# Kernel tuning notes

Hardware: AMD Instinct MI355X
Metric: run time of the kernel (lower is better)

Reference implementation:

```python
import jax, jax.numpy as jnp
import numpy as np

CL = 32      # config.cl (latent width)
NOBJ = 32    # config.num_obj
N = 1024     # batch


def _linear_params(key, fan_in, fan_out):
    w = jax.random.normal(key, (fan_in, fan_out), dtype=jnp.float32) / np.sqrt(fan_in)
    b = jnp.full((fan_out,), 0.1, dtype=jnp.float32)
    return w, b


def setup_inputs() -> dict:
    key = jax.random.key(0)
    keys = jax.random.split(key, 16)
    inp = {"s": jax.random.normal(keys[0], (N, NOBJ, CL // 2), dtype=jnp.float32)}
    specs = [
        ("state_enc", [(CL // 2, CL)]),
        ("self", [(CL, CL), (CL, CL)]),
        ("rel", [(2 * CL + 1, 2 * CL), (2 * CL, CL), (CL, CL)]),
        ("att", [(2 * CL + 1, 2 * CL), (2 * CL, CL), (CL, 1)]),
        ("aff", [(CL, CL), (CL, CL), (CL, CL)]),
        ("out", [(2 * CL, CL), (CL, CL)]),
    ]
    k = 1
    for name, shapes in specs:
        for j, (fi, fo) in enumerate(shapes):
            w, b = _linear_params(keys[k], fi, fo)
            k += 1
            if len(shapes) == 1:
                inp[name + "_w"], inp[name + "_b"] = w, b
            else:
                inp[name + "_w" + str(j)], inp[name + "_b" + str(j)] = w, b
    inp["core_idx"] = 0
    return inp


def _forward(s, state_enc_w, state_enc_b,
             self_w0, self_b0, self_w1, self_b1,
             rel_w0, rel_b0, rel_w1, rel_b1, rel_w2, rel_b2,
             att_w0, att_b0, att_w1, att_b1, att_w2, att_b2,
             aff_w0, aff_b0, aff_w1, aff_b1, aff_w2, aff_b2,
             out_w0, out_b0, out_w1, out_b1):
    # state encoding; keep raw (x, y) positions in the first 2 channels
    enc = s @ state_enc_w + state_enc_b                      # (n, o, cl)
    s2 = jnp.concatenate([s[..., :2], enc[..., 2:]], axis=-1)  # (n, o, cl)

    # self dynamics (residual MLP)
    h1 = jax.nn.relu(s2 @ self_w0 + self_b0)
    self_dyn = h1 @ self_w1 + self_b1 + h1                   # (n, o, cl)

    # pairwise squared distance over first two channels
    pos = s2[..., :2]
    diff = pos[:, :, None, :] - pos[:, None, :, :]           # (n, o, o, 2)
    dist = jnp.sum(diff * diff, axis=-1)                     # (n, o, o)

    # first layer of the edge MLPs applied to cat(obj_i, obj_j, dist) without
    # materializing the (n, o, o, 2cl+1) concat: split weight into W_i|W_j|w_d
    def pair_first(W, b):
        a = s2 @ W[:CL]                                      # (n, o, H)
        c = s2 @ W[CL:2 * CL]                                # (n, o, H)
        return a[:, :, None, :] + c[:, None, :, :] + dist[..., None] * W[2 * CL] + b

    # relation core (residual on last layer)
    rel1 = jax.nn.relu(pair_first(rel_w0, rel_b0))           # (n, o, o, 2cl)
    rel2 = jax.nn.relu(rel1 @ rel_w1 + rel_b1)               # (n, o, o, cl)
    rel_f = rel2 @ rel_w2 + rel_b2 + rel2                    # (n, o, o, cl)

    # attention net -> exp (unnormalized attention)
    att = jax.nn.relu(pair_first(att_w0, att_b0))
    att = jax.nn.relu(att @ att_w1 + att_b1)
    att = jnp.exp(att @ att_w2 + att_b2)                     # (n, o, o, 1)

    diag_mask = (1.0 - jnp.eye(NOBJ, dtype=s2.dtype))[None, :, :, None]
    rel_dyn = jnp.sum(rel_f * diag_mask * att, axis=2)       # (n, o, cl)

    dyn = self_dyn + rel_dyn

    # affector (tanh residual MLP)
    aff1 = jnp.tanh(dyn @ aff_w0 + aff_b0)
    aff2 = jnp.tanh(aff1 @ aff_w1 + aff_b1) + aff1
    aff3 = aff2 @ aff_w2 + aff_b2

    # output head
    aff_s = jnp.concatenate([aff3, s2], axis=-1)             # (n, o, 2cl)
    o1 = jnp.tanh(aff_s @ out_w0 + out_b0)
    result = o1 @ out_w1 + out_b1 + o1                       # (n, o, cl)
    return result


def reference(s, state_enc_w, state_enc_b,
              self_w0, self_b0, self_w1, self_b1,
              rel_w0, rel_b0, rel_w1, rel_b1, rel_w2, rel_b2,
              att_w0, att_b0, att_w1, att_b1, att_w2, att_b2,
              aff_w0, aff_b0, aff_w1, aff_b1, aff_w2, aff_b2,
              out_w0, out_b0, out_w1, out_b1, core_idx):
    # core_idx selects one of 3 identical cores in the original; only core 0
    # is materialized here (forward uses a single core).
    del core_idx
    return _forward(s, state_enc_w, state_enc_b,
                    self_w0, self_b0, self_w1, self_b1,
                    rel_w0, rel_b0, rel_w1, rel_b1, rel_w2, rel_b2,
                    att_w0, att_b0, att_w1, att_b1, att_w2, att_b2,
                    aff_w0, aff_b0, aff_w1, aff_b1, aff_w2, aff_b2,
                    out_w0, out_b0, out_w1, out_b1)
```

## Files before the change

kernel.cpp:

```cpp
#include <hip/hip_runtime.h>
#include <stdint.h>


enum : int {
  ENC_W  = 0,     ENC_B  = 512,
  SELF_W0 = 544,  SELF_B0 = 1568, SELF_W1 = 1600, SELF_B1 = 2624,
  REL_W0 = 2656,  REL_B0 = 6816,  REL_W1 = 6880,  REL_B1 = 8928,
  REL_W2 = 8960,  REL_B2 = 9984,
  ATT_W0 = 10016, ATT_B0 = 14176, ATT_W1 = 14240, ATT_B1 = 16288,
  ATT_W2 = 16320, ATT_B2 = 16352,
  AFF_W0 = 16356, AFF_B0 = 17380, AFF_W1 = 17412, AFF_B1 = 18436,
  AFF_W2 = 18468, AFF_B2 = 19492,
  OUT_W0 = 19524, OUT_B0 = 21572, OUT_W1 = 21604, OUT_B1 = 22628,
  W_FLAG = 22660,
  W_TOTAL = 22661
};

__device__ __forceinline__ float bf2f(uint16_t h) {
  union { uint32_t u; float f; } v; v.u = ((uint32_t)h) << 16; return v.f;
}
__device__ __forceinline__ uint16_t f2bf(float f) {
  union { float f; uint32_t u; } v; v.f = f;
  uint32_t r = (v.u + 0x7fffu + ((v.u >> 16) & 1u)) >> 16;
  return (uint16_t)r;
}

struct ConvArgs {
  const void* src[28];
  const uint32_t* probe;
  int size[28];
  int off[28];
};

__global__ void dyn_conv_kernel(ConvArgs a, float* __restrict__ W) {
  const int t = blockIdx.x;
  const bool is_fp32 = (*a.probe == 0x3DCCCCCDu);
  const int cnt = a.size[t];
  float* d = W + a.off[t];
  if (is_fp32) {
    const float* s = (const float*)a.src[t];
    for (int e = threadIdx.x; e < cnt; e += blockDim.x) d[e] = s[e];
  } else {
    const uint16_t* s = (const uint16_t*)a.src[t];
    for (int e = threadIdx.x; e < cnt; e += blockDim.x) d[e] = bf2f(s[e]);
  }
  if (t == 0 && threadIdx.x == 0) W[W_FLAG] = is_fp32 ? 1.f : 0.f;
}

struct ArenaPair {
  float ar[32][68];
  float cr[32][68];
  float aa[32][68];
  float ca[32][68];
  float wdr[64];
  float wda[64];
};
struct ArenaPost {
  float rd[32][36];
  float t1[32][36];
  float t2[32][36];
};
struct ArenaEarly {
  float s[32][16];
  float h1[32][33];
};
union ArenaU {
  ArenaPair a;
  ArenaPost b;
  ArenaEarly c;
};

__global__ __launch_bounds__(256, 2) void dyn_main_kernel(
    const void* __restrict__ Sv,
    const float* __restrict__ Wf,
    void* __restrict__ OUTv)
{
  __shared__ __align__(16) ArenaU u;
  __shared__ float sh_s2[32][33];
  __shared__ float sh_dist[32][33];
  __shared__ float sh_sd[32][33];
  __shared__ __align__(16) float sh_rw1[2048];
  __shared__ __align__(16) float sh_aw1[2048];
  __shared__ float sh_misc[100];

  const int tid = threadIdx.x;
  const int n   = blockIdx.x;
  const int i8  = tid >> 3;
  const int l8  = tid & 7;
  const int m0  = l8 << 2;

  const bool is_fp32 = (Wf[W_FLAG] != 0.f);

  {
    const int e = tid * 2;
    if (is_fp32) {
      const float* sp = (const float*)Sv + (size_t)n * 512;
      u.c.s[e >> 4][e & 15]             = sp[e];
      u.c.s[(e + 1) >> 4][(e + 1) & 15] = sp[e + 1];
    } else {
      const uint16_t* sp = (const uint16_t*)Sv + (size_t)n * 512;
      u.c.s[e >> 4][e & 15]             = bf2f(sp[e]);
      u.c.s[(e + 1) >> 4][(e + 1) & 15] = bf2f(sp[e + 1]);
    }
  }
  __syncthreads();

  {
    float e0 = Wf[ENC_B + m0 + 0], e1 = Wf[ENC_B + m0 + 1];
    float e2 = Wf[ENC_B + m0 + 2], e3 = Wf[ENC_B + m0 + 3];
    #pragma unroll
    for (int c = 0; c < 16; ++c) {
      const float sc = u.c.s[i8][c];
      const float4 w = *(const float4*)&Wf[ENC_W + c * 32 + m0];
      e0 = fmaf(sc, w.x, e0); e1 = fmaf(sc, w.y, e1);
      e2 = fmaf(sc, w.z, e2); e3 = fmaf(sc, w.w, e3);
    }
    if (m0 == 0) { e0 = u.c.s[i8][0]; e1 = u.c.s[i8][1]; }
    sh_s2[i8][m0 + 0] = e0; sh_s2[i8][m0 + 1] = e1;
    sh_s2[i8][m0 + 2] = e2; sh_s2[i8][m0 + 3] = e3;
  }
  __syncthreads();

  {
    const float xi = sh_s2[i8][0], yi = sh_s2[i8][1];
    #pragma unroll
    for (int q = 0; q < 4; ++q) {
      const int j = m0 + q;
      const float dx = xi - sh_s2[j][0];
      const float dy = yi - sh_s2[j][1];
      sh_dist[i8][j] = dx * dx + dy * dy;
    }
  }
  {
    float a0 = Wf[SELF_B0 + m0 + 0], a1 = Wf[SELF_B0 + m0 + 1];
    float a2 = Wf[SELF_B0 + m0 + 2], a3 = Wf[SELF_B0 + m0 + 3];
    #pragma unroll
    for (int k = 0; k < 32; ++k) {
      const float x = sh_s2[i8][k];
      const float4 w = *(const float4*)&Wf[SELF_W0 + k * 32 + m0];
      a0 = fmaf(x, w.x, a0); a1 = fmaf(x, w.y, a1);
      a2 = fmaf(x, w.z, a2); a3 = fmaf(x, w.w, a3);
    }
    u.c.h1[i8][m0 + 0] = fmaxf(a0, 0.f); u.c.h1[i8][m0 + 1] = fmaxf(a1, 0.f);
    u.c.h1[i8][m0 + 2] = fmaxf(a2, 0.f); u.c.h1[i8][m0 + 3] = fmaxf(a3, 0.f);
  }
  __syncthreads();

  {
    float a0 = Wf[SELF_B1 + m0 + 0], a1 = Wf[SELF_B1 + m0 + 1];
    float a2 = Wf[SELF_B1 + m0 + 2], a3 = Wf[SELF_B1 + m0 + 3];
    #pragma unroll
    for (int k = 0; k < 32; ++k) {
      const float x = u.c.h1[i8][k];
      const float4 w = *(const float4*)&Wf[SELF_W1 + k * 32 + m0];
      a0 = fmaf(x, w.x, a0); a1 = fmaf(x, w.y, a1);
      a2 = fmaf(x, w.z, a2); a3 = fmaf(x, w.w, a3);
    }
    sh_sd[i8][m0 + 0] = a0 + u.c.h1[i8][m0 + 0];
    sh_sd[i8][m0 + 1] = a1 + u.c.h1[i8][m0 + 1];
    sh_sd[i8][m0 + 2] = a2 + u.c.h1[i8][m0 + 2];
    sh_sd[i8][m0 + 3] = a3 + u.c.h1[i8][m0 + 3];
  }
  __syncthreads();

  if (tid < 64)        u.a.wdr[tid]      = Wf[REL_W0 + 64 * 64 + tid];
  else if (tid < 128)  u.a.wda[tid - 64] = Wf[ATT_W0 + 64 * 64 + (tid - 64)];
  {
    #pragma unroll
    for (int q = 0; q < 2; ++q) {
      const int i4 = tid + q * 256;
      ((float4*)sh_rw1)[i4] = *(const float4*)&Wf[REL_W1 + i4 * 4];
      ((float4*)sh_aw1)[i4] = *(const float4*)&Wf[ATT_W1 + i4 * 4];
    }
    if (tid < 97)
      sh_misc[tid] = Wf[tid < 32 ? REL_B1 + tid
                      : tid < 64 ? ATT_B1 + (tid - 32)
                      : tid < 96 ? ATT_W2 + (tid - 64) : ATT_B2];
  }
  {
    const int task = tid >> 1;
    const int arr  = task >> 5;
    const int row  = task & 31;
    const int k0   = (tid & 1) * 32;
    const float* wb; const float* bb; float bs;
    if (arr == 0)      { wb = Wf + REL_W0;        bb = Wf + REL_B0 + k0; bs = 1.f; }
    else if (arr == 1) { wb = Wf + REL_W0 + 2048; bb = Wf + REL_B0;      bs = 0.f; }
    else if (arr == 2) { wb = Wf + ATT_W0;        bb = Wf + ATT_B0 + k0; bs = 1.f; }
    else               { wb = Wf + ATT_W0 + 2048; bb = Wf + ATT_B0;      bs = 0.f; }
    float acc[32];
    #pragma unroll
    for (int kk = 0; kk < 32; ++kk) acc[kk] = bs * bb[kk];
    for (int c = 0; c < 32; ++c) {
      const float sc = sh_s2[row][c];
      const float* w = wb + c * 64 + k0;
      #pragma unroll
      for (int kk = 0; kk < 32; kk += 4) {
        const float4 wv = *(const float4*)&w[kk];
        acc[kk + 0] = fmaf(sc, wv.x, acc[kk + 0]);
        acc[kk + 1] = fmaf(sc, wv.y, acc[kk + 1]);
        acc[kk + 2] = fmaf(sc, wv.z, acc[kk + 2]);
        acc[kk + 3] = fmaf(sc, wv.w, acc[kk + 3]);
      }
    }
    float* dst = (arr == 0) ? &u.a.ar[row][k0] : (arr == 1) ? &u.a.cr[row][k0]
               : (arr == 2) ? &u.a.aa[row][k0] : &u.a.ca[row][k0];
    #pragma unroll
    for (int kk = 0; kk < 32; kk += 4)
      *(float4*)&dst[kk] = make_float4(acc[kk], acc[kk + 1], acc[kk + 2], acc[kk + 3]);
  }
  __syncthreads();

  float E = 0.f;
  float g[32];
  #pragma unroll
  for (int m = 0; m < 32; ++m) g[m] = 0.f;

  const float4* Aa = (const float4*)&u.a.aa[i8][0];
  const float4* Da = (const float4*)&u.a.wda[0];
  const float4* Ar = (const float4*)&u.a.ar[i8][0];
  const float4* Dr = (const float4*)&u.a.wdr[0];

  #pragma unroll 1
  for (int p = 0; p < 4; ++p) {
    const int j = l8 + 8 * p;
    const float d = sh_dist[i8][j];
    const float4* Ca = (const float4*)&u.a.ca[j][0];
    const float4* Cr = (const float4*)&u.a.cr[j][0];
    float v[32];

    #pragma unroll
    for (int m = 0; m < 32; ++m) v[m] = sh_misc[32 + m];
    #pragma unroll 1
    for (int kq = 0; kq < 16; ++kq) {
      const float4 av = Aa[kq], cv = Ca[kq], wv = Da[kq];
      const float x0 = fmaxf(fmaf(d, wv.x, av.x + cv.x), 0.f);
      const float x1 = fmaxf(fmaf(d, wv.y, av.y + cv.y), 0.f);
      const float x2 = fmaxf(fmaf(d, wv.z, av.z + cv.z), 0.f);
      const float x3 = fmaxf(fmaf(d, wv.w, av.w + cv.w), 0.f);
      const float4* wb = (const float4*)sh_aw1 + kq * 32;
      #pragma unroll
      for (int mq = 0; mq < 8; ++mq) {
        const float4 w0 = wb[mq], w1 = wb[8 + mq], w2 = wb[16 + mq], w3 = wb[24 + mq];
        float t;
        t = fmaf(x0, w0.x, v[mq*4+0]); t = fmaf(x1, w1.x, t);
        t = fmaf(x2, w2.x, t);         v[mq*4+0] = fmaf(x3, w3.x, t);
        t = fmaf(x0, w0.y, v[mq*4+1]); t = fmaf(x1, w1.y, t);
        t = fmaf(x2, w2.y, t);         v[mq*4+1] = fmaf(x3, w3.y, t);
        t = fmaf(x0, w0.z, v[mq*4+2]); t = fmaf(x1, w1.z, t);
        t = fmaf(x2, w2.z, t);         v[mq*4+2] = fmaf(x3, w3.z, t);
        t = fmaf(x0, w0.w, v[mq*4+3]); t = fmaf(x1, w1.w, t);
        t = fmaf(x2, w2.w, t);         v[mq*4+3] = fmaf(x3, w3.w, t);
      }
    }
    float lg0 = sh_misc[96], lg1 = 0.f, lg2 = 0.f, lg3 = 0.f;
    #pragma unroll
    for (int k = 0; k < 32; k += 4) {
      lg0 = fmaf(fmaxf(v[k + 0], 0.f), sh_misc[64 + k + 0], lg0);
      lg1 = fmaf(fmaxf(v[k + 1], 0.f), sh_misc[64 + k + 1], lg1);
      lg2 = fmaf(fmaxf(v[k + 2], 0.f), sh_misc[64 + k + 2], lg2);
      lg3 = fmaf(fmaxf(v[k + 3], 0.f), sh_misc[64 + k + 3], lg3);
    }
    const float e = (j == i8) ? 0.f : expf((lg0 + lg1) + (lg2 + lg3));
    E += e;

    #pragma unroll
    for (int m = 0; m < 32; ++m) v[m] = sh_misc[m];
    #pragma unroll 1
    for (int kq = 0; kq < 16; ++kq) {
      const float4 av = Ar[kq], cv = Cr[kq], wv = Dr[kq];
      const float x0 = fmaxf(fmaf(d, wv.x, av.x + cv.x), 0.f);
      const float x1 = fmaxf(fmaf(d, wv.y, av.y + cv.y), 0.f);
      const float x2 = fmaxf(fmaf(d, wv.z, av.z + cv.z), 0.f);
      const float x3 = fmaxf(fmaf(d, wv.w, av.w + cv.w), 0.f);
      const float4* wb = (const float4*)sh_rw1 + kq * 32;
      #pragma unroll
      for (int mq = 0; mq < 8; ++mq) {
        const float4 w0 = wb[mq], w1 = wb[8 + mq], w2 = wb[16 + mq], w3 = wb[24 + mq];
        float t;
        t = fmaf(x0, w0.x, v[mq*4+0]); t = fmaf(x1, w1.x, t);
        t = fmaf(x2, w2.x, t);         v[mq*4+0] = fmaf(x3, w3.x, t);
        t = fmaf(x0, w0.y, v[mq*4+1]); t = fmaf(x1, w1.y, t);
        t = fmaf(x2, w2.y, t);         v[mq*4+1] = fmaf(x3, w3.y, t);
        t = fmaf(x0, w0.z, v[mq*4+2]); t = fmaf(x1, w1.z, t);
        t = fmaf(x2, w2.z, t);         v[mq*4+2] = fmaf(x3, w3.z, t);
        t = fmaf(x0, w0.w, v[mq*4+3]); t = fmaf(x1, w1.w, t);
        t = fmaf(x2, w2.w, t);         v[mq*4+3] = fmaf(x3, w3.w, t);
      }
    }
    #pragma unroll
    for (int m = 0; m < 32; ++m)
      g[m] = fmaf(e, fmaxf(v[m], 0.f), g[m]);
  }

  #pragma unroll
  for (int m = 0; m < 32; ++m) {
    float vv = g[m];
    vv += __shfl_xor(vv, 1);
    vv += __shfl_xor(vv, 2);
    vv += __shfl_xor(vv, 4);
    g[m] = vv;
  }
  E += __shfl_xor(E, 1);
  E += __shfl_xor(E, 2);
  E += __shfl_xor(E, 4);
  __syncthreads();
  if (l8 == 0) {
    #pragma unroll
    for (int q = 0; q < 8; ++q)
      *(float4*)&u.b.t1[i8][q * 4] =
          make_float4(g[q * 4], g[q * 4 + 1], g[q * 4 + 2], g[q * 4 + 3]);
    u.b.t1[i8][32] = E;
  }
  __syncthreads();

  {
    const float Ei = u.b.t1[i8][32];
    float a0 = fmaf(Ei, Wf[REL_B2 + m0 + 0], u.b.t1[i8][m0 + 0]);
    float a1 = fmaf(Ei, Wf[REL_B2 + m0 + 1], u.b.t1[i8][m0 + 1]);
    float a2 = fmaf(Ei, Wf[REL_B2 + m0 + 2], u.b.t1[i8][m0 + 2]);
    float a3 = fmaf(Ei, Wf[REL_B2 + m0 + 3], u.b.t1[i8][m0 + 3]);
    #pragma unroll
    for (int k = 0; k < 32; ++k) {
      const float x = u.b.t1[i8][k];
      const float4 w = *(const float4*)&Wf[REL_W2 + k * 32 + m0];
      a0 = fmaf(x, w.x, a0); a1 = fmaf(x, w.y, a1);
      a2 = fmaf(x, w.z, a2); a3 = fmaf(x, w.w, a3);
    }
    __syncthreads();
    u.b.rd[i8][m0 + 0] = a0; u.b.rd[i8][m0 + 1] = a1;
    u.b.rd[i8][m0 + 2] = a2; u.b.rd[i8][m0 + 3] = a3;
  }
  __syncthreads();

  {
    float a0 = Wf[AFF_B0 + m0 + 0], a1 = Wf[AFF_B0 + m0 + 1];
    float a2 = Wf[AFF_B0 + m0 + 2], a3 = Wf[AFF_B0 + m0 + 3];
    #pragma unroll
    for (int k = 0; k < 32; ++k) {
      const float x = sh_sd[i8][k] + u.b.rd[i8][k];
      const float4 w = *(const float4*)&Wf[AFF_W0 + k * 32 + m0];
      a0 = fmaf(x, w.x, a0); a1 = fmaf(x, w.y, a1);
      a2 = fmaf(x, w.z, a2); a3 = fmaf(x, w.w, a3);
    }
    u.b.t1[i8][m0 + 0] = tanhf(a0); u.b.t1[i8][m0 + 1] = tanhf(a1);
    u.b.t1[i8][m0 + 2] = tanhf(a2); u.b.t1[i8][m0 + 3] = tanhf(a3);
  }
  __syncthreads();

  {
    float a0 = Wf[AFF_B1 + m0 + 0], a1 = Wf[AFF_B1 + m0 + 1];
    float a2 = Wf[AFF_B1 + m0 + 2], a3 = Wf[AFF_B1 + m0 + 3];
    #pragma unroll
    for (int k = 0; k < 32; ++k) {
      const float x = u.b.t1[i8][k];
      const float4 w = *(const float4*)&Wf[AFF_W1 + k * 32 + m0];
      a0 = fmaf(x, w.x, a0); a1 = fmaf(x, w.y, a1);
      a2 = fmaf(x, w.z, a2); a3 = fmaf(x, w.w, a3);
    }
    u.b.t2[i8][m0 + 0] = tanhf(a0) + u.b.t1[i8][m0 + 0];
    u.b.t2[i8][m0 + 1] = tanhf(a1) + u.b.t1[i8][m0 + 1];
    u.b.t2[i8][m0 + 2] = tanhf(a2) + u.b.t1[i8][m0 + 2];
    u.b.t2[i8][m0 + 3] = tanhf(a3) + u.b.t1[i8][m0 + 3];
  }
  __syncthreads();

  {
    float a0 = Wf[AFF_B2 + m0 + 0], a1 = Wf[AFF_B2 + m0 + 1];
    float a2 = Wf[AFF_B2 + m0 + 2], a3 = Wf[AFF_B2 + m0 + 3];
    #pragma unroll
    for (int k = 0; k < 32; ++k) {
      const float x = u.b.t2[i8][k];
      const float4 w = *(const float4*)&Wf[AFF_W2 + k * 32 + m0];
      a0 = fmaf(x, w.x, a0); a1 = fmaf(x, w.y, a1);
      a2 = fmaf(x, w.z, a2); a3 = fmaf(x, w.w, a3);
    }
    u.b.t1[i8][m0 + 0] = a0; u.b.t1[i8][m0 + 1] = a1;
    u.b.t1[i8][m0 + 2] = a2; u.b.t1[i8][m0 + 3] = a3;
  }
  __syncthreads();

  {
    float a0 = Wf[OUT_B0 + m0 + 0], a1 = Wf[OUT_B0 + m0 + 1];
    float a2 = Wf[OUT_B0 + m0 + 2], a3 = Wf[OUT_B0 + m0 + 3];
    #pragma unroll
    for (int k = 0; k < 32; ++k) {
      const float x1 = u.b.t1[i8][k];
      const float4 wa = *(const float4*)&Wf[OUT_W0 + k * 32 + m0];
      a0 = fmaf(x1, wa.x, a0); a1 = fmaf(x1, wa.y, a1);
      a2 = fmaf(x1, wa.z, a2); a3 = fmaf(x1, wa.w, a3);
      const float x2 = sh_s2[i8][k];
      const float4 wbv = *(const float4*)&Wf[OUT_W0 + (32 + k) * 32 + m0];
      a0 = fmaf(x2, wbv.x, a0); a1 = fmaf(x2, wbv.y, a1);
      a2 = fmaf(x2, wbv.z, a2); a3 = fmaf(x2, wbv.w, a3);
    }
    u.b.t2[i8][m0 + 0] = tanhf(a0); u.b.t2[i8][m0 + 1] = tanhf(a1);
    u.b.t2[i8][m0 + 2] = tanhf(a2); u.b.t2[i8][m0 + 3] = tanhf(a3);
  }
  __syncthreads();

  {
    float a0 = Wf[OUT_B1 + m0 + 0], a1 = Wf[OUT_B1 + m0 + 1];
    float a2 = Wf[OUT_B1 + m0 + 2], a3 = Wf[OUT_B1 + m0 + 3];
    #pragma unroll
    for (int k = 0; k < 32; ++k) {
      const float x = u.b.t2[i8][k];
      const float4 w = *(const float4*)&Wf[OUT_W1 + k * 32 + m0];
      a0 = fmaf(x, w.x, a0); a1 = fmaf(x, w.y, a1);
      a2 = fmaf(x, w.z, a2); a3 = fmaf(x, w.w, a3);
    }
    a0 += u.b.t2[i8][m0 + 0]; a1 += u.b.t2[i8][m0 + 1];
    a2 += u.b.t2[i8][m0 + 2]; a3 += u.b.t2[i8][m0 + 3];
    const size_t idx = (size_t)n * 1024 + i8 * 32 + m0;
    if (is_fp32) {
      *(float4*)&((float*)OUTv)[idx] = make_float4(a0, a1, a2, a3);
    } else {
      ushort4 r;
      r.x = f2bf(a0); r.y = f2bf(a1); r.z = f2bf(a2); r.w = f2bf(a3);
      *(ushort4*)&((uint16_t*)OUTv)[idx] = r;
    }
  }
}

extern "C" void kernel_launch(void* const* d_in, const int* in_sizes, int n_in,
                              void* d_out, int out_size, void* d_ws, size_t ws_size,
                              hipStream_t stream) {
  (void)in_sizes; (void)n_in; (void)out_size; (void)ws_size;
  static const int sizes[28] = {
    512, 32, 1024, 32, 1024, 32,
    4160, 64, 2048, 32, 1024, 32,
    4160, 64, 2048, 32, 32, 1,
    1024, 32, 1024, 32, 1024, 32,
    2048, 32, 1024, 32};
  static const int offs[28] = {
    ENC_W, ENC_B, SELF_W0, SELF_B0, SELF_W1, SELF_B1,
    REL_W0, REL_B0, REL_W1, REL_B1, REL_W2, REL_B2,
    ATT_W0, ATT_B0, ATT_W1, ATT_B1, ATT_W2, ATT_B2,
    AFF_W0, AFF_B0, AFF_W1, AFF_B1, AFF_W2, AFF_B2,
    OUT_W0, OUT_B0, OUT_W1, OUT_B1};

  ConvArgs ca;
  for (int i = 0; i < 28; ++i) {
    ca.src[i]  = d_in[1 + i];
    ca.size[i] = sizes[i];
    ca.off[i]  = offs[i];
  }
  ca.probe = (const uint32_t*)d_in[2];
  float* W = (float*)d_ws;
  hipLaunchKernelGGL(dyn_conv_kernel, dim3(28), dim3(256), 0, stream, ca, W);
  hipLaunchKernelGGL(dyn_main_kernel, dim3(1024), dim3(256), 0, stream,
                     d_in[0], (const float*)W, d_out);
}
```

Baseline: 383.4 us.

## Split attention and relation phases to halve shared memory and raise occupancy

The fused per-pair loop that computed attention and relation MLPs together is split into two sequential phases. They share one W1 buffer and one pair of precomputed A/C arrays, which roughly halves the LDS footprint, and launch bounds rise from 2 to 4 blocks per CU. This targets low occupancy from LDS and register pressure. In exchange it adds extra barriers, reloads weights between phases, and keeps four exp values live across phases, and the tighter register cap may cause spills.

```diff
diff --git a/kernel.cpp b/kernel.cpp
--- a/kernel.cpp
+++ b/kernel.cpp
@@ -48,12 +48,8 @@
 }
 
 struct ArenaPair {
-  float ar[32][68];
-  float cr[32][68];
-  float aa[32][68];
-  float ca[32][68];
-  float wdr[64];
-  float wda[64];
+  float pa[32][68];
+  float pc[32][68];
 };
 struct ArenaPost {
   float rd[32][36];
@@ -70,7 +66,7 @@
   ArenaEarly c;
 };
 
-__global__ __launch_bounds__(256, 2) void dyn_main_kernel(
+__global__ __launch_bounds__(256, 4) void dyn_main_kernel(
     const void* __restrict__ Sv,
     const float* __restrict__ Wf,
     void* __restrict__ OUTv)
@@ -79,8 +75,9 @@
   __shared__ float sh_s2[32][33];
   __shared__ float sh_dist[32][33];
   __shared__ float sh_sd[32][33];
-  __shared__ __align__(16) float sh_rw1[2048];
-  __shared__ __align__(16) float sh_aw1[2048];
+  __shared__ float sh_wdr[64];
+  __shared__ float sh_wda[64];
+  __shared__ __align__(16) float shW1[2048];
   __shared__ float sh_misc[100];
 
   const int tid = threadIdx.x;
@@ -163,38 +160,21 @@
   }
   __syncthreads();
 
-  if (tid < 64)        u.a.wdr[tid]      = Wf[REL_W0 + 64 * 64 + tid];
-  else if (tid < 128)  u.a.wda[tid - 64] = Wf[ATT_W0 + 64 * 64 + (tid - 64)];
-  {
-    #pragma unroll
-    for (int q = 0; q < 2; ++q) {
-      const int i4 = tid + q * 256;
-      ((float4*)sh_rw1)[i4] = *(const float4*)&Wf[REL_W1 + i4 * 4];
-      ((float4*)sh_aw1)[i4] = *(const float4*)&Wf[ATT_W1 + i4 * 4];
-    }
-    if (tid < 97)
-      sh_misc[tid] = Wf[tid < 32 ? REL_B1 + tid
-                      : tid < 64 ? ATT_B1 + (tid - 32)
-                      : tid < 96 ? ATT_W2 + (tid - 64) : ATT_B2];
-  }
-  {
-    const int task = tid >> 1;
-    const int arr  = task >> 5;
-    const int row  = task & 31;
-    const int k0   = (tid & 1) * 32;
-    const float* wb; const float* bb; float bs;
-    if (arr == 0)      { wb = Wf + REL_W0;        bb = Wf + REL_B0 + k0; bs = 1.f; }
-    else if (arr == 1) { wb = Wf + REL_W0 + 2048; bb = Wf + REL_B0;      bs = 0.f; }
-    else if (arr == 2) { wb = Wf + ATT_W0;        bb = Wf + ATT_B0 + k0; bs = 1.f; }
-    else               { wb = Wf + ATT_W0 + 2048; bb = Wf + ATT_B0;      bs = 0.f; }
-    float acc[32];
-    #pragma unroll
-    for (int kk = 0; kk < 32; ++kk) acc[kk] = bs * bb[kk];
+  auto precompute_ac = [&](int W0base, int B0base) {
+    const int arr = tid >> 7;
+    const int row = (tid >> 2) & 31;
+    const int k0  = (tid & 3) * 16;
+    const float* bb = Wf + B0base + k0;
+    const float bs = (arr == 0) ? 1.f : 0.f;
+    float acc[16];
+    #pragma unroll
+    for (int kk = 0; kk < 16; ++kk) acc[kk] = bs * bb[kk];
+    const float* wb = Wf + W0base + arr * 2048 + k0;
     for (int c = 0; c < 32; ++c) {
       const float sc = sh_s2[row][c];
-      const float* w = wb + c * 64 + k0;
+      const float* w = wb + c * 64;
       #pragma unroll
-      for (int kk = 0; kk < 32; kk += 4) {
+      for (int kk = 0; kk < 16; kk += 4) {
         const float4 wv = *(const float4*)&w[kk];
         acc[kk + 0] = fmaf(sc, wv.x, acc[kk + 0]);
         acc[kk + 1] = fmaf(sc, wv.y, acc[kk + 1]);
@@ -202,45 +182,44 @@
         acc[kk + 3] = fmaf(sc, wv.w, acc[kk + 3]);
       }
     }
-    float* dst = (arr == 0) ? &u.a.ar[row][k0] : (arr == 1) ? &u.a.cr[row][k0]
-               : (arr == 2) ? &u.a.aa[row][k0] : &u.a.ca[row][k0];
-    #pragma unroll
-    for (int kk = 0; kk < 32; kk += 4)
-      *(float4*)&dst[kk] = make_float4(acc[kk], acc[kk + 1], acc[kk + 2], acc[kk + 3]);
-  }
-  __syncthreads();
-
-  float E = 0.f;
-  float g[32];
-  #pragma unroll
-  for (int m = 0; m < 32; ++m) g[m] = 0.f;
-
-  const float4* Aa = (const float4*)&u.a.aa[i8][0];
-  const float4* Da = (const float4*)&u.a.wda[0];
-  const float4* Ar = (const float4*)&u.a.ar[i8][0];
-  const float4* Dr = (const float4*)&u.a.wdr[0];
-
-  #pragma unroll 1
-  for (int p = 0; p < 4; ++p) {
+    float* dst = (arr == 0) ? &u.a.pa[row][k0] : &u.a.pc[row][k0];
+    #pragma unroll
+    for (int kk = 0; kk < 16; kk += 4)
+      *(float4*)&dst[kk] = make_float4(acc[kk], acc[kk+1], acc[kk+2], acc[kk+3]);
+  };
+
+  if (tid < 64)        sh_wdr[tid]      = Wf[REL_W0 + 64 * 64 + tid];
+  else if (tid < 128)  sh_wda[tid - 64] = Wf[ATT_W0 + 64 * 64 + (tid - 64)];
+  ((float4*)shW1)[tid]       = *(const float4*)&Wf[ATT_W1 + tid * 4];
+  ((float4*)shW1)[tid + 256] = *(const float4*)&Wf[ATT_W1 + (tid + 256) * 4];
+  if (tid < 97)
+    sh_misc[tid] = Wf[tid < 32 ? REL_B1 + tid
+                    : tid < 64 ? ATT_B1 + (tid - 32)
+                    : tid < 96 ? ATT_W2 + (tid - 64) : ATT_B2];
+  precompute_ac(ATT_W0, ATT_B0);
+  __syncthreads();
+
+  auto att_pair = [&](int p) -> float {
+    asm volatile("" ::: "memory");
     const int j = l8 + 8 * p;
     const float d = sh_dist[i8][j];
-    const float4* Ca = (const float4*)&u.a.ca[j][0];
-    const float4* Cr = (const float4*)&u.a.cr[j][0];
+    const float4* A = (const float4*)&u.a.pa[i8][0];
+    const float4* C = (const float4*)&u.a.pc[j][0];
+    const float4* D = (const float4*)&sh_wda[0];
     float v[32];
-
     #pragma unroll
     for (int m = 0; m < 32; ++m) v[m] = sh_misc[32 + m];
     #pragma unroll 1
     for (int kq = 0; kq < 16; ++kq) {
-      const float4 av = Aa[kq], cv = Ca[kq], wv = Da[kq];
+      const float4 av = A[kq], cv = C[kq], wv = D[kq];
       const float x0 = fmaxf(fmaf(d, wv.x, av.x + cv.x), 0.f);
       const float x1 = fmaxf(fmaf(d, wv.y, av.y + cv.y), 0.f);
       const float x2 = fmaxf(fmaf(d, wv.z, av.z + cv.z), 0.f);
       const float x3 = fmaxf(fmaf(d, wv.w, av.w + cv.w), 0.f);
-      const float4* wb = (const float4*)sh_aw1 + kq * 32;
+      const float4* wb = (const float4*)shW1 + kq * 32;
       #pragma unroll
       for (int mq = 0; mq < 8; ++mq) {
-        const float4 w0 = wb[mq], w1 = wb[8 + mq], w2 = wb[16 + mq], w3 = wb[24 + mq];
+        const float4 w0 = wb[mq], w1 = wb[8+mq], w2 = wb[16+mq], w3 = wb[24+mq];
         float t;
         t = fmaf(x0, w0.x, v[mq*4+0]); t = fmaf(x1, w1.x, t);
         t = fmaf(x2, w2.x, t);         v[mq*4+0] = fmaf(x3, w3.x, t);
@@ -252,30 +231,54 @@
         t = fmaf(x2, w2.w, t);         v[mq*4+3] = fmaf(x3, w3.w, t);
       }
     }
-    float lg0 = sh_misc[96], lg1 = 0.f, lg2 = 0.f, lg3 = 0.f;
+    float s0 = sh_misc[96], s1 = 0.f, s2 = 0.f, s3 = 0.f;
     #pragma unroll
     for (int k = 0; k < 32; k += 4) {
-      lg0 = fmaf(fmaxf(v[k + 0], 0.f), sh_misc[64 + k + 0], lg0);
-      lg1 = fmaf(fmaxf(v[k + 1], 0.f), sh_misc[64 + k + 1], lg1);
-      lg2 = fmaf(fmaxf(v[k + 2], 0.f), sh_misc[64 + k + 2], lg2);
-      lg3 = fmaf(fmaxf(v[k + 3], 0.f), sh_misc[64 + k + 3], lg3);
-    }
-    const float e = (j == i8) ? 0.f : expf((lg0 + lg1) + (lg2 + lg3));
-    E += e;
-
+      s0 = fmaf(fmaxf(v[k + 0], 0.f), sh_misc[64 + k + 0], s0);
+      s1 = fmaf(fmaxf(v[k + 1], 0.f), sh_misc[64 + k + 1], s1);
+      s2 = fmaf(fmaxf(v[k + 2], 0.f), sh_misc[64 + k + 2], s2);
+      s3 = fmaf(fmaxf(v[k + 3], 0.f), sh_misc[64 + k + 3], s3);
+    }
+    const float lg = (s0 + s1) + (s2 + s3);
+    return (j == i8) ? 0.f : expf(lg);
+  };
+  const float e0 = att_pair(0);
+  const float e1 = att_pair(1);
+  const float e2 = att_pair(2);
+  const float e3 = att_pair(3);
+  float E = (e0 + e1) + (e2 + e3);
+  __syncthreads();
+
+  ((float4*)shW1)[tid]       = *(const float4*)&Wf[REL_W1 + tid * 4];
+  ((float4*)shW1)[tid + 256] = *(const float4*)&Wf[REL_W1 + (tid + 256) * 4];
+  precompute_ac(REL_W0, REL_B0);
+  __syncthreads();
+
+  float g[32];
+  #pragma unroll
+  for (int m = 0; m < 32; ++m) g[m] = 0.f;
+
+  auto rel_pair = [&](int p, float e) {
+    asm volatile("" ::: "memory");
+    const int j = l8 + 8 * p;
+    const float d = sh_dist[i8][j];
+    const float4* A = (const float4*)&u.a.pa[i8][0];
+    const float4* C = (const float4*)&u.a.pc[j][0];
+    const float4* D = (const float4*)&sh_wdr[0];
+    float v[32];
     #pragma unroll
     for (int m = 0; m < 32; ++m) v[m] = sh_misc[m];
     #pragma unroll 1
     for (int kq = 0; kq < 16; ++kq) {
-      const float4 av = Ar[kq], cv = Cr[kq], wv = Dr[kq];
+      const float4 av = A[kq], cv = C[kq], wv = D[kq];
       const float x0 = fmaxf(fmaf(d, wv.x, av.x + cv.x), 0.f);
       const float x1 = fmaxf(fmaf(d, wv.y, av.y + cv.y), 0.f);
       const float x2 = fmaxf(fmaf(d, wv.z, av.z + cv.z), 0.f);
       const float x3 = fmaxf(fmaf(d, wv.w, av.w + cv.w), 0.f);
-      const float4* wb = (const float4*)sh_rw1 + kq * 32;
+      const float4* wb = (const float4*)shW1 + kq * 32;
       #pragma unroll
       for (int mq = 0; mq < 8; ++mq) {
-        const float4 w0 = wb[mq], w1 = wb[8 + mq], w2 = wb[16 + mq], w3 = wb[24 + mq];
+        const float4 w0 = wb[mq], w1 = wb[8+mq], w2 = wb[16+mq], w3 = wb[24+mq];
         float t;
         t = fmaf(x0, w0.x, v[mq*4+0]); t = fmaf(x1, w1.x, t);
         t = fmaf(x2, w2.x, t);         v[mq*4+0] = fmaf(x3, w3.x, t);
@@ -290,7 +293,11 @@
     #pragma unroll
     for (int m = 0; m < 32; ++m)
       g[m] = fmaf(e, fmaxf(v[m], 0.f), g[m]);
-  }
+  };
+  rel_pair(0, e0);
+  rel_pair(1, e1);
+  rel_pair(2, e2);
+  rel_pair(3, e3);
 
   #pragma unroll
   for (int m = 0; m < 32; ++m) {
```

After: 501.5 us. +30.8%, slower.
